# Performance work log

Measured on AMD Instinct MI355X. Metric: run time of the kernel, lower is better.

## Reference

```python
import jax, jax.numpy as jnp
import numpy as np

B, L, F, H = 16, 4096, 512, 512


def setup_inputs() -> dict:
    key = jax.random.key(0)
    ks = jax.random.split(key, 8)
    return {
        "x": jax.random.normal(ks[0], (B, L, F), dtype=jnp.float32),
        "B_real": jax.random.normal(ks[1], (F, H), dtype=jnp.float32),
        "B_img": jax.random.normal(ks[2], (F, H), dtype=jnp.float32),
        "nu": jax.random.normal(ks[3], (H,), dtype=jnp.float32),
        "theta": jax.random.uniform(ks[4], (H,), dtype=jnp.float32),
        "delta": jax.random.uniform(ks[5], (H,), dtype=jnp.float32),
        "h0_real": jax.random.normal(ks[6], (H,), dtype=jnp.float32),
        "h0_img": jax.random.normal(ks[7], (H,), dtype=jnp.float32),
    }


def reference(x, B_real, B_img, nu, theta, delta, h0_real, h0_img):
    # Diagonal complex recurrence: h_t = lam * h_{t-1} + delta * (B x_t),
    # h_0 = h0_real + i h0_img, returning Re(h_1..h_L).
    lam = jnp.exp(-jnp.exp(nu) + 1j * theta)  # (H,) complex64
    # Input projection (compute-bound GEMMs), then scale by delta.
    Bx = (jnp.matmul(x, B_real) + 1j * jnp.matmul(x, B_img)) * delta  # (B,L,H)

    bsz, seqlen, hid = Bx.shape
    lam_b = jnp.broadcast_to(lam, Bx.shape)

    def combine(e1, e2):
        a1, b1 = e1
        a2, b2 = e2
        return (a1 * a2, a2 * b1 + b2)

    # Log-depth associative scan over the sequence axis (equiv. to the
    # torch Blelchon-style doubling loop; front zero-padding is a no-op).
    _, h = jax.lax.associative_scan(combine, (lam_b, Bx), axis=1)

    # h0 contribution: lam^{t+1} * h0 for t = 0..L-1
    lam_pow = jnp.cumprod(jnp.broadcast_to(lam, (seqlen, hid)), axis=0)  # (L,H)
    h0 = h0_real + 1j * h0_img  # (H,)
    h0_contrib = lam_pow[None, :, :] * h0[None, None, :]  # (1,L,H)
    return (h + h0_contrib).real
```

## Files before the change

kernel.cpp:

```cpp
#include <hip/hip_runtime.h>

typedef __attribute__((ext_vector_type(8))) short s16x8;
typedef __attribute__((ext_vector_type(4))) float f32x4;

constexpr int B_ = 16;
constexpr int L_ = 4096;
constexpr int F_ = 512;
constexpr int H_ = 512;
constexpr int CT = 32;
constexpr int NC = L_ / CT;
constexpr int NCP = NC / 2;
constexpr int XROW = 520;

constexpr size_t WSOUT_OFF   = (size_t)9 << 20;
constexpr size_t WSOUT_BYTES = (size_t)B_ * L_ * H_ * 2;

static __device__ __forceinline__ unsigned short f2bf(float f) {
  union { float f; unsigned u; } v; v.f = f;
  unsigned r = (v.u + 0x7FFFu + ((v.u >> 16) & 1u)) >> 16;
  return (unsigned short)r;
}
static __device__ __forceinline__ float bf2f(unsigned short s) {
  union { unsigned u; float f; } v; v.u = ((unsigned)s) << 16;
  return v.f;
}

__global__ void bprep_kernel(const float* __restrict__ BR, const float* __restrict__ BI,
                             s16x8* __restrict__ BpR, s16x8* __restrict__ BpI) {
  int ht = blockIdx.x >> 4;
  int fk = blockIdx.x & 15;
  int l  = threadIdx.x;
  int h  = ht * 16 + (l & 15);
  int f0 = fk * 32 + (l >> 4) * 8;
  s16x8 r, im;
#pragma unroll
  for (int j = 0; j < 8; ++j) {
    r[j]  = (short)f2bf(BR[(size_t)(f0 + j) * H_ + h]);
    im[j] = (short)f2bf(BI[(size_t)(f0 + j) * H_ + h]);
  }
  int idx = (ht * 16 + fk) * 64 + l;
  BpR[idx] = r;
  BpI[idx] = im;
}

template <bool FUSED>
__global__ __launch_bounds__(512, 2) void gemm_scan_kernel(
    const float* __restrict__ x,
    const s16x8* __restrict__ BpR, const s16x8* __restrict__ BpI,
    const float* __restrict__ nu, const float* __restrict__ theta,
    const float* __restrict__ delta,
    float* __restrict__ out, unsigned short* __restrict__ wsout,
    float* __restrict__ ER, float* __restrict__ EI) {
  __shared__ __align__(16) unsigned short xs[2 * CT * XROW];

  const int hs   = blockIdx.x;
  const int cy   = blockIdx.y;
  const int b    = blockIdx.z;
  const int tid  = threadIdx.x;
  const int lane = tid & 63;
  const int w    = tid >> 6;
  const int g    = lane >> 4;
  const int cl   = lane & 15;

  const float* xp = x + (size_t)(b * L_ + cy * 2 * CT) * F_;
#pragma unroll
  for (int i = 0; i < 8; ++i) {
    int row = i * 8 + w;
    int col = lane * 8;
    const float4 v0 = *(const float4*)(xp + row * F_ + col);
    const float4 v1 = *(const float4*)(xp + row * F_ + col + 4);
    s16x8 pk;
    pk[0] = (short)f2bf(v0.x); pk[1] = (short)f2bf(v0.y);
    pk[2] = (short)f2bf(v0.z); pk[3] = (short)f2bf(v0.w);
    pk[4] = (short)f2bf(v1.x); pk[5] = (short)f2bf(v1.y);
    pk[6] = (short)f2bf(v1.z); pk[7] = (short)f2bf(v1.w);
    *(s16x8*)(xs + row * XROW + col) = pk;
  }
  __syncthreads();

  f32x4 accR[2][2][2], accI[2][2][2];
#pragma unroll
  for (int cc = 0; cc < 2; ++cc)
#pragma unroll
    for (int tt = 0; tt < 2; ++tt)
#pragma unroll
      for (int j = 0; j < 2; ++j) {
        accR[cc][tt][j] = (f32x4){0.f, 0.f, 0.f, 0.f};
        accI[cc][tt][j] = (f32x4){0.f, 0.f, 0.f, 0.f};
      }

#pragma unroll 4
  for (int fk = 0; fk < 16; ++fk) {
    s16x8 a[2][2];
#pragma unroll
    for (int cc = 0; cc < 2; ++cc)
#pragma unroll
      for (int tt = 0; tt < 2; ++tt)
        a[cc][tt] = *(const s16x8*)(xs + (cc * 32 + tt * 16 + cl) * XROW + fk * 32 + g * 8);
#pragma unroll
    for (int j = 0; j < 2; ++j) {
      int ht = hs * 16 + w * 2 + j;
      s16x8 br = BpR[(ht * 16 + fk) * 64 + lane];
      s16x8 bi = BpI[(ht * 16 + fk) * 64 + lane];
#pragma unroll
      for (int cc = 0; cc < 2; ++cc)
#pragma unroll
        for (int tt = 0; tt < 2; ++tt) {
          accR[cc][tt][j] = __builtin_amdgcn_mfma_f32_16x16x32_bf16(a[cc][tt], br, accR[cc][tt][j], 0, 0, 0);
          accI[cc][tt][j] = __builtin_amdgcn_mfma_f32_16x16x32_bf16(a[cc][tt], bi, accI[cc][tt][j], 0, 0, 0);
        }
    }
  }

#pragma unroll
  for (int j = 0; j < 2; ++j) {
    const int h = (hs * 16 + w * 2 + j) * 16 + cl;
    const float dl = delta[h];
    const float mag = __expf(-__expf(nu[h]));
    const float th  = theta[h];
    const float lr = mag * __cosf(th), li = mag * __sinf(th);
    const float l2r = lr*lr - li*li,     l2i = 2.f*lr*li;
    const float l3r = l2r*lr - l2i*li,   l3i = l2r*li + l2i*lr;
    const float l4r = l2r*l2r - l2i*l2i, l4i = 2.f*l2r*l2i;
    const float l8r = l4r*l4r - l4i*l4i, l8i = 2.f*l4r*l4i;
    const float l12r = l8r*l4r - l8i*l4i, l12i = l8r*l4i + l8i*l4r;
    const float l16r = l8r*l8r - l8i*l8i, l16i = 2.f*l8r*l8i;
    const float m4r = (g==0)?1.f:((g==1)?l4r:((g==2)?l8r:l12r));
    const float m4i = (g==0)?0.f:((g==1)?l4i:((g==2)?l8i:l12i));

#pragma unroll
    for (int cc = 0; cc < 2; ++cc) {
      const int c = cy * 2 + cc;
      float carryR = 0.f, carryI = 0.f;
      float* opf = out + (size_t)(b * L_ + c * CT) * H_ + h;
      unsigned short* opw = FUSED ? (wsout + (size_t)(b * L_ + c * CT) * H_ + h) : nullptr;

#pragma unroll
      for (int tt = 0; tt < 2; ++tt) {
        float lsR[4], lsI[4];
        float sR = 0.f, sI = 0.f;
#pragma unroll
        for (int r = 0; r < 4; ++r) {
          float uR = dl * accR[cc][tt][j][r], uI = dl * accI[cc][tt][j][r];
          float nR = lr * sR - li * sI + uR;
          float nI = lr * sI + li * sR + uI;
          sR = nR; sI = nI; lsR[r] = sR; lsI[r] = sI;
        }
        float qR = __shfl(sR, (lane - 16) & 63, 64);
        float qI = __shfl(sI, (lane - 16) & 63, 64);
        float I1R = (g >= 1) ? sR + l4r*qR - l4i*qI : sR;
        float I1I = (g >= 1) ? sI + l4r*qI + l4i*qR : sI;
        float q2R = __shfl(I1R, (lane - 32) & 63, 64);
        float q2I = __shfl(I1I, (lane - 32) & 63, 64);
        float I2R = (g >= 2) ? I1R + l8r*q2R - l8i*q2I : I1R;
        float I2I = (g >= 2) ? I1I + l8r*q2I + l8i*q2R : I1I;
        float eR = __shfl(I2R, (lane - 16) & 63, 64);
        float eI = __shfl(I2I, (lane - 16) & 63, 64);
        eR = (g >= 1) ? eR : 0.f;
        eI = (g >= 1) ? eI : 0.f;
        float incR = m4r * carryR - m4i * carryI + eR;
        float incI = m4r * carryI + m4i * carryR + eI;
        {
          float o0 = lsR[0] + lr  * incR - li  * incI;
          float o1 = lsR[1] + l2r * incR - l2i * incI;
          float o2 = lsR[2] + l3r * incR - l3i * incI;
          float o3 = lsR[3] + l4r * incR - l4i * incI;
          if (FUSED) {
            opw[(size_t)(tt * 16 + g * 4 + 0) * H_] = f2bf(o0);
            opw[(size_t)(tt * 16 + g * 4 + 1) * H_] = f2bf(o1);
            opw[(size_t)(tt * 16 + g * 4 + 2) * H_] = f2bf(o2);
            opw[(size_t)(tt * 16 + g * 4 + 3) * H_] = f2bf(o3);
          } else {
            opf[(size_t)(tt * 16 + g * 4 + 0) * H_] = o0;
            opf[(size_t)(tt * 16 + g * 4 + 1) * H_] = o1;
            opf[(size_t)(tt * 16 + g * 4 + 2) * H_] = o2;
            opf[(size_t)(tt * 16 + g * 4 + 3) * H_] = o3;
          }
        }
        float fR = __shfl(I2R, 48 | cl, 64);
        float fI = __shfl(I2I, 48 | cl, 64);
        float ncR = fR + l16r * carryR - l16i * carryI;
        float ncI = fI + l16r * carryI + l16i * carryR;
        carryR = ncR; carryI = ncI;
      }
      if (g == 0) {
        size_t eidx = (size_t)(b * NC + c) * H_ + h;
        ER[eidx] = carryR;
        EI[eidx] = carryI;
      }
    }
  }
}

__global__ void combine_kernel(const float* __restrict__ nu, const float* __restrict__ theta,
                               const float* __restrict__ h0r, const float* __restrict__ h0i,
                               float* __restrict__ ER, float* __restrict__ EI) {
  int gg = blockIdx.x * blockDim.x + threadIdx.x;
  int b = gg >> 9;
  int h = gg & (H_ - 1);
  float mag = __expf(-__expf(nu[h]));
  float lr  = mag * __cosf(theta[h]);
  float li  = mag * __sinf(theta[h]);
  float pr = lr, pi = li;
#pragma unroll
  for (int s = 0; s < 5; ++s) {
    float nr = pr * pr - pi * pi;
    float ni = 2.f * pr * pi;
    pr = nr; pi = ni;
  }
  float sR = h0r[h], sI = h0i[h];
  for (int c0 = 0; c0 < NC; c0 += 8) {
    float tR[8], tI[8];
#pragma unroll
    for (int k = 0; k < 8; ++k) {
      size_t idx = (size_t)(b * NC + c0 + k) * H_ + h;
      tR[k] = ER[idx]; tI[k] = EI[idx];
    }
#pragma unroll
    for (int k = 0; k < 8; ++k) {
      size_t idx = (size_t)(b * NC + c0 + k) * H_ + h;
      ER[idx] = sR; EI[idx] = sI;
      float nR = pr * sR - pi * sI + tR[k];
      float nI = pr * sI + pi * sR + tI[k];
      sR = nR; sI = nI;
    }
  }
}

__global__ void fixup_kernel(const float* __restrict__ nu, const float* __restrict__ theta,
                             const float* __restrict__ ER, const float* __restrict__ EI,
                             float* __restrict__ out) {
  int c = blockIdx.x, b = blockIdx.y;
  int h = threadIdx.x;
  size_t idx = (size_t)(b * NC + c) * H_ + h;
  float hR = ER[idx], hI = EI[idx];
  float mag = __expf(-__expf(nu[h]));
  float lr  = mag * __cosf(theta[h]);
  float li  = mag * __sinf(theta[h]);
  float pr = lr, pi = li;
  float* op = out + (size_t)(b * L_ + c * CT) * H_ + h;
#pragma unroll 4
  for (int k = 0; k < CT; ++k) {
    op[(size_t)k * H_] += pr * hR - pi * hI;
    float nr = pr * lr - pi * li;
    float ni = pr * li + pi * lr;
    pr = nr; pi = ni;
  }
}

__global__ void fixup_fused_kernel(const float* __restrict__ nu, const float* __restrict__ theta,
                                   const float* __restrict__ ER, const float* __restrict__ EI,
                                   const unsigned short* __restrict__ wsout,
                                   float* __restrict__ out) {
  int c = blockIdx.x, b = blockIdx.y;
  int h = threadIdx.x;
  size_t idx = (size_t)(b * NC + c) * H_ + h;
  float hR = ER[idx], hI = EI[idx];
  float mag = __expf(-__expf(nu[h]));
  float lr  = mag * __cosf(theta[h]);
  float li  = mag * __sinf(theta[h]);
  float pr = lr, pi = li;
  size_t base = (size_t)(b * L_ + c * CT) * H_ + h;
  const unsigned short* wp = wsout + base;
  float* op = out + base;
#pragma unroll 4
  for (int k = 0; k < CT; ++k) {
    op[(size_t)k * H_] = bf2f(wp[(size_t)k * H_]) + (pr * hR - pi * hI);
    float nr = pr * lr - pi * li;
    float ni = pr * li + pi * lr;
    pr = nr; pi = ni;
  }
}

extern "C" void kernel_launch(void* const* d_in, const int* in_sizes, int n_in,
                              void* d_out, int out_size, void* d_ws, size_t ws_size,
                              hipStream_t stream) {
  const float* x   = (const float*)d_in[0];
  const float* BR  = (const float*)d_in[1];
  const float* BI  = (const float*)d_in[2];
  const float* nu  = (const float*)d_in[3];
  const float* th  = (const float*)d_in[4];
  const float* dl  = (const float*)d_in[5];
  const float* h0r = (const float*)d_in[6];
  const float* h0i = (const float*)d_in[7];
  float* out = (float*)d_out;

  char* wsc = (char*)d_ws;
  s16x8* BpR = (s16x8*)(wsc);
  s16x8* BpI = (s16x8*)(wsc + (512 << 10));
  float* ER  = (float*)(wsc + (1 << 20));
  float* EI  = (float*)(wsc + (1 << 20) + (size_t)B_ * NC * H_ * 4);
  unsigned short* wsout = (unsigned short*)(wsc + WSOUT_OFF);
  const bool fused = ws_size >= WSOUT_OFF + WSOUT_BYTES;

  hipLaunchKernelGGL(bprep_kernel, dim3(512), dim3(64), 0, stream, BR, BI, BpR, BpI);
  if (fused) {
    hipLaunchKernelGGL((gemm_scan_kernel<true>), dim3(2, NCP, B_), dim3(512), 0, stream,
                       x, BpR, BpI, nu, th, dl, out, wsout, ER, EI);
    hipLaunchKernelGGL(combine_kernel, dim3(16), dim3(512), 0, stream, nu, th, h0r, h0i, ER, EI);
    hipLaunchKernelGGL(fixup_fused_kernel, dim3(NC, B_), dim3(512), 0, stream,
                       nu, th, ER, EI, wsout, out);
  } else {
    hipLaunchKernelGGL((gemm_scan_kernel<false>), dim3(2, NCP, B_), dim3(512), 0, stream,
                       x, BpR, BpI, nu, th, dl, out, wsout, ER, EI);
    hipLaunchKernelGGL(combine_kernel, dim3(16), dim3(512), 0, stream, nu, th, h0r, h0i, ER, EI);
    hipLaunchKernelGGL(fixup_kernel, dim3(NC, B_), dim3(512), 0, stream, nu, th, ER, EI, out);
  }
}
```

Measured before the change: 172.4 us.

## Keep B tiles in registers and stream sequence chunks with register prefetch

```diff
diff --git a/kernel.cpp b/kernel.cpp
--- a/kernel.cpp
+++ b/kernel.cpp
@@ -9,7 +9,7 @@
 constexpr int H_ = 512;
 constexpr int CT = 32;
 constexpr int NC = L_ / CT;
-constexpr int NCP = NC / 2;
+constexpr int KC = 16;
 constexpr int XROW = 520;
 
 constexpr size_t WSOUT_OFF   = (size_t)9 << 20;
@@ -44,17 +44,17 @@
 }
 
 template <bool FUSED>
-__global__ __launch_bounds__(512, 2) void gemm_scan_kernel(
+__global__ __launch_bounds__(512, 1) void gemm_scan_kernel(
     const float* __restrict__ x,
     const s16x8* __restrict__ BpR, const s16x8* __restrict__ BpI,
     const float* __restrict__ nu, const float* __restrict__ theta,
     const float* __restrict__ delta,
     float* __restrict__ out, unsigned short* __restrict__ wsout,
     float* __restrict__ ER, float* __restrict__ EI) {
-  __shared__ __align__(16) unsigned short xs[2 * CT * XROW];
-
-  const int hs   = blockIdx.x;
-  const int cy   = blockIdx.y;
+  __shared__ __align__(16) unsigned short xs[CT * XROW];
+
+  const int ls   = blockIdx.x;
+  const int hq   = blockIdx.y;
   const int b    = blockIdx.z;
   const int tid  = threadIdx.x;
   const int lane = tid & 63;
@@ -62,75 +62,86 @@
   const int g    = lane >> 4;
   const int cl   = lane & 15;
 
-  const float* xp = x + (size_t)(b * L_ + cy * 2 * CT) * F_;
-#pragma unroll
-  for (int i = 0; i < 8; ++i) {
+  const int ht = hq * 8 + w;
+  const int h  = ht * 16 + cl;
+
+  s16x8 Brg[16], Big[16];
+#pragma unroll
+  for (int fk = 0; fk < 16; ++fk) {
+    Brg[fk] = BpR[(ht * 16 + fk) * 64 + lane];
+    Big[fk] = BpI[(ht * 16 + fk) * 64 + lane];
+  }
+
+  const float dl = delta[h];
+  const float mag = __expf(-__expf(nu[h]));
+  const float thv = theta[h];
+  const float lr = mag * __cosf(thv), li = mag * __sinf(thv);
+  const float l2r = lr*lr - li*li,     l2i = 2.f*lr*li;
+  const float l3r = l2r*lr - l2i*li,   l3i = l2r*li + l2i*lr;
+  const float l4r = l2r*l2r - l2i*l2i, l4i = 2.f*l2r*l2i;
+  const float l8r = l4r*l4r - l4i*l4i, l8i = 2.f*l4r*l4i;
+  const float l12r = l8r*l4r - l8i*l4i, l12i = l8r*l4i + l8i*l4r;
+  const float l16r = l8r*l8r - l8i*l8i, l16i = 2.f*l8r*l8i;
+  const float m4r = (g==0)?1.f:((g==1)?l4r:((g==2)?l8r:l12r));
+  const float m4i = (g==0)?0.f:((g==1)?l4i:((g==2)?l8i:l12i));
+
+  const float* xbase = x + (size_t)(b * L_ + ls * KC * CT) * F_;
+
+  float4 pv[4][2];
+#pragma unroll
+  for (int i = 0; i < 4; ++i) {
     int row = i * 8 + w;
-    int col = lane * 8;
-    const float4 v0 = *(const float4*)(xp + row * F_ + col);
-    const float4 v1 = *(const float4*)(xp + row * F_ + col + 4);
-    s16x8 pk;
-    pk[0] = (short)f2bf(v0.x); pk[1] = (short)f2bf(v0.y);
-    pk[2] = (short)f2bf(v0.z); pk[3] = (short)f2bf(v0.w);
-    pk[4] = (short)f2bf(v1.x); pk[5] = (short)f2bf(v1.y);
-    pk[6] = (short)f2bf(v1.z); pk[7] = (short)f2bf(v1.w);
-    *(s16x8*)(xs + row * XROW + col) = pk;
-  }
-  __syncthreads();
-
-  f32x4 accR[2][2][2], accI[2][2][2];
-#pragma unroll
-  for (int cc = 0; cc < 2; ++cc)
-#pragma unroll
-    for (int tt = 0; tt < 2; ++tt)
-#pragma unroll
-      for (int j = 0; j < 2; ++j) {
-        accR[cc][tt][j] = (f32x4){0.f, 0.f, 0.f, 0.f};
-        accI[cc][tt][j] = (f32x4){0.f, 0.f, 0.f, 0.f};
+    pv[i][0] = *(const float4*)(xbase + (size_t)row * F_ + lane * 8);
+    pv[i][1] = *(const float4*)(xbase + (size_t)row * F_ + lane * 8 + 4);
+  }
+
+#pragma unroll 1
+  for (int k = 0; k < KC; ++k) {
+    __syncthreads();
+
+#pragma unroll
+    for (int i = 0; i < 4; ++i) {
+      int row = i * 8 + w;
+      s16x8 pk;
+      pk[0] = (short)f2bf(pv[i][0].x); pk[1] = (short)f2bf(pv[i][0].y);
+      pk[2] = (short)f2bf(pv[i][0].z); pk[3] = (short)f2bf(pv[i][0].w);
+      pk[4] = (short)f2bf(pv[i][1].x); pk[5] = (short)f2bf(pv[i][1].y);
+      pk[6] = (short)f2bf(pv[i][1].z); pk[7] = (short)f2bf(pv[i][1].w);
+      *(s16x8*)(&xs[row * XROW + lane * 8]) = pk;
+    }
+    __syncthreads();
+
+    if (k + 1 < KC) {
+      const float* xq = xbase + (size_t)(k + 1) * CT * F_;
+#pragma unroll
+      for (int i = 0; i < 4; ++i) {
+        int row = i * 8 + w;
+        pv[i][0] = *(const float4*)(xq + (size_t)row * F_ + lane * 8);
+        pv[i][1] = *(const float4*)(xq + (size_t)row * F_ + lane * 8 + 4);
       }
-
-#pragma unroll 4
-  for (int fk = 0; fk < 16; ++fk) {
-    s16x8 a[2][2];
-#pragma unroll
-    for (int cc = 0; cc < 2; ++cc)
+    }
+
+    f32x4 accR[2], accI[2];
+#pragma unroll
+    for (int tt = 0; tt < 2; ++tt) {
+      accR[tt] = (f32x4){0.f, 0.f, 0.f, 0.f};
+      accI[tt] = (f32x4){0.f, 0.f, 0.f, 0.f};
+    }
+#pragma unroll
+    for (int fk = 0; fk < 16; ++fk) {
+      s16x8 a[2];
 #pragma unroll
       for (int tt = 0; tt < 2; ++tt)
-        a[cc][tt] = *(const s16x8*)(xs + (cc * 32 + tt * 16 + cl) * XROW + fk * 32 + g * 8);
-#pragma unroll
-    for (int j = 0; j < 2; ++j) {
-      int ht = hs * 16 + w * 2 + j;
-      s16x8 br = BpR[(ht * 16 + fk) * 64 + lane];
-      s16x8 bi = BpI[(ht * 16 + fk) * 64 + lane];
-#pragma unroll
-      for (int cc = 0; cc < 2; ++cc)
-#pragma unroll
-        for (int tt = 0; tt < 2; ++tt) {
-          accR[cc][tt][j] = __builtin_amdgcn_mfma_f32_16x16x32_bf16(a[cc][tt], br, accR[cc][tt][j], 0, 0, 0);
-          accI[cc][tt][j] = __builtin_amdgcn_mfma_f32_16x16x32_bf16(a[cc][tt], bi, accI[cc][tt][j], 0, 0, 0);
-        }
-    }
-  }
-
-#pragma unroll
-  for (int j = 0; j < 2; ++j) {
-    const int h = (hs * 16 + w * 2 + j) * 16 + cl;
-    const float dl = delta[h];
-    const float mag = __expf(-__expf(nu[h]));
-    const float th  = theta[h];
-    const float lr = mag * __cosf(th), li = mag * __sinf(th);
-    const float l2r = lr*lr - li*li,     l2i = 2.f*lr*li;
-    const float l3r = l2r*lr - l2i*li,   l3i = l2r*li + l2i*lr;
-    const float l4r = l2r*l2r - l2i*l2i, l4i = 2.f*l2r*l2i;
-    const float l8r = l4r*l4r - l4i*l4i, l8i = 2.f*l4r*l4i;
-    const float l12r = l8r*l4r - l8i*l4i, l12i = l8r*l4i + l8i*l4r;
-    const float l16r = l8r*l8r - l8i*l8i, l16i = 2.f*l8r*l8i;
-    const float m4r = (g==0)?1.f:((g==1)?l4r:((g==2)?l8r:l12r));
-    const float m4i = (g==0)?0.f:((g==1)?l4i:((g==2)?l8i:l12i));
-
-#pragma unroll
-    for (int cc = 0; cc < 2; ++cc) {
-      const int c = cy * 2 + cc;
+        a[tt] = *(const s16x8*)(&xs[(tt * 16 + cl) * XROW + fk * 32 + g * 8]);
+#pragma unroll
+      for (int tt = 0; tt < 2; ++tt) {
+        accR[tt] = __builtin_amdgcn_mfma_f32_16x16x32_bf16(a[tt], Brg[fk], accR[tt], 0, 0, 0);
+        accI[tt] = __builtin_amdgcn_mfma_f32_16x16x32_bf16(a[tt], Big[fk], accI[tt], 0, 0, 0);
+      }
+    }
+
+    const int c = ls * KC + k;
+    {
       float carryR = 0.f, carryI = 0.f;
       float* opf = out + (size_t)(b * L_ + c * CT) * H_ + h;
       unsigned short* opw = FUSED ? (wsout + (size_t)(b * L_ + c * CT) * H_ + h) : nullptr;
@@ -141,7 +152,7 @@
         float sR = 0.f, sI = 0.f;
 #pragma unroll
         for (int r = 0; r < 4; ++r) {
-          float uR = dl * accR[cc][tt][j][r], uI = dl * accI[cc][tt][j][r];
+          float uR = dl * accR[tt][r], uI = dl * accI[tt][r];
           float nR = lr * sR - li * sI + uR;
           float nI = lr * sI + li * sR + uI;
           sR = nR; sI = nI; lsR[r] = sR; lsI[r] = sI;
@@ -295,13 +306,13 @@
 
   hipLaunchKernelGGL(bprep_kernel, dim3(512), dim3(64), 0, stream, BR, BI, BpR, BpI);
   if (fused) {
-    hipLaunchKernelGGL((gemm_scan_kernel<true>), dim3(2, NCP, B_), dim3(512), 0, stream,
+    hipLaunchKernelGGL((gemm_scan_kernel<true>), dim3(8, 4, B_), dim3(512), 0, stream,
                        x, BpR, BpI, nu, th, dl, out, wsout, ER, EI);
     hipLaunchKernelGGL(combine_kernel, dim3(16), dim3(512), 0, stream, nu, th, h0r, h0i, ER, EI);
     hipLaunchKernelGGL(fixup_fused_kernel, dim3(NC, B_), dim3(512), 0, stream,
                        nu, th, ER, EI, wsout, out);
   } else {
-    hipLaunchKernelGGL((gemm_scan_kernel<false>), dim3(2, NCP, B_), dim3(512), 0, stream,
+    hipLaunchKernelGGL((gemm_scan_kernel<false>), dim3(8, 4, B_), dim3(512), 0, stream,
                        x, BpR, BpI, nu, th, dl, out, wsout, ER, EI);
     hipLaunchKernelGGL(combine_kernel, dim3(16), dim3(512), 0, stream, nu, th, h0r, h0i, ER, EI);
     hipLaunchKernelGGL(fixup_kernel, dim3(NC, B_), dim3(512), 0, stream, nu, th, ER, EI, out);
```

Result: faster. 157.6 us (-8.6%).
